# Optimization experiments

Hardware: AMD Instinct MI355X
Metric: run time of the kernel (lower is better)

The kernel has to match this reference:

```python
import jax, jax.numpy as jnp
import numpy as np

N, E, D, H = 4096, 131072, 256, 8
DH = D // H  # head dim = 32


def layer_norm(x, g, b, eps=1e-5):
    mu = jnp.mean(x, axis=-1, keepdims=True)
    var = jnp.var(x, axis=-1, keepdims=True)
    return (x - mu) * jax.lax.rsqrt(var + eps) * g + b


def mlp2(x, w1, b1, w2, b2):
    # Linear -> GELU(exact) -> Linear (dropout is identity at inference)
    return jax.nn.gelu(x @ w1 + b1, approximate=False) @ w2 + b2


def setup_inputs() -> dict:
    key = jax.random.key(0)
    ks = iter(jax.random.split(key, 32))
    s = 0.02
    d = {
        'x': jax.random.normal(next(ks), (N, D), jnp.float32),
        'edge_index': jax.random.randint(next(ks), (2, E), 0, N, jnp.int32),
        'edge_attr': jax.random.normal(next(ks), (E, D), jnp.float32),
        # GINE eps
        'eps': jnp.zeros((1,), jnp.float32),
        # edge MLP (Linear weights stored [in, out])
        'e_w1': jax.random.normal(next(ks), (D, D), jnp.float32) * s,
        'e_b1': jnp.zeros((D,), jnp.float32),
        'e_w2': jax.random.normal(next(ks), (D, D), jnp.float32) * s,
        'e_b2': jnp.zeros((D,), jnp.float32),
        # update MLP
        'u_w1': jax.random.normal(next(ks), (D, D), jnp.float32) * s,
        'u_b1': jnp.zeros((D,), jnp.float32),
        'u_w2': jax.random.normal(next(ks), (D, D), jnp.float32) * s,
        'u_b2': jnp.zeros((D,), jnp.float32),
        # LayerNorms
        'ln_local_g': jnp.ones((D,), jnp.float32), 'ln_local_b': jnp.zeros((D,), jnp.float32),
        'ln_global_g': jnp.ones((D,), jnp.float32), 'ln_global_b': jnp.zeros((D,), jnp.float32),
        'ln_ffn_g': jnp.ones((D,), jnp.float32), 'ln_ffn_b': jnp.zeros((D,), jnp.float32),
        # MHA projections ([in, out])
        'wq': jax.random.normal(next(ks), (D, D), jnp.float32) * s,
        'wk': jax.random.normal(next(ks), (D, D), jnp.float32) * s,
        'wv': jax.random.normal(next(ks), (D, D), jnp.float32) * s,
        'bq': jnp.zeros((D,), jnp.float32), 'bk': jnp.zeros((D,), jnp.float32), 'bv': jnp.zeros((D,), jnp.float32),
        'wo': jax.random.normal(next(ks), (D, D), jnp.float32) * s,
        'bo': jnp.zeros((D,), jnp.float32),
        # FFN
        'f_w1': jax.random.normal(next(ks), (D, 4 * D), jnp.float32) * s,
        'f_b1': jnp.zeros((4 * D,), jnp.float32),
        'f_w2': jax.random.normal(next(ks), (4 * D, D), jnp.float32) * s,
        'f_b2': jnp.zeros((D,), jnp.float32),
    }
    return d


def reference(x, edge_index, edge_attr, eps,
              e_w1, e_b1, e_w2, e_b2, u_w1, u_b1, u_w2, u_b2,
              ln_local_g, ln_local_b, ln_global_g, ln_global_b, ln_ffn_g, ln_ffn_b,
              wq, wk, wv, bq, bk, bv, wo, bo,
              f_w1, f_b1, f_w2, f_b2):
    src, dst = edge_index[0], edge_index[1]
    n = x.shape[0]

    # ---- local GINE conv on pre-normed features ----
    h = layer_norm(x, ln_local_g, ln_local_b)
    messages = mlp2(h[src] + edge_attr, e_w1, e_b1, e_w2, e_b2)  # [E, D]
    aggregated = jax.ops.segment_sum(messages, dst, num_segments=n)  # [N, D]
    local = mlp2((1.0 + eps) * h + aggregated, u_w1, u_b1, u_w2, u_b2)
    x = x + local

    # ---- global multihead self-attention over all nodes ----
    g = layer_norm(x, ln_global_g, ln_global_b)
    q = (g @ wq + bq).reshape(n, H, DH)
    k = (g @ wk + bk).reshape(n, H, DH)
    v = (g @ wv + bv).reshape(n, H, DH)
    scores = jnp.einsum('nhd,mhd->hnm', q, k) / jnp.sqrt(jnp.float32(DH))
    attn = jax.nn.softmax(scores, axis=-1)
    ctx = jnp.einsum('hnm,mhd->nhd', attn, v).reshape(n, D)
    x = x + (ctx @ wo + bo)

    # ---- FFN ----
    x = x + mlp2(layer_norm(x, ln_ffn_g, ln_ffn_b), f_w1, f_b1, f_w2, f_b2)
    return x
```

## Files before the change

### kernel.cpp

```cpp
#include <hip/hip_runtime.h>
#include <math.h>

#define N_NODES 4096
#define N_EDGES 131072
#define XPAD    264

using bf16x8 = __attribute__((ext_vector_type(8))) __bf16;
using f32x4  = __attribute__((ext_vector_type(4))) float;
typedef unsigned short u16;

__device__ __forceinline__ u16 f2bf(float f) {
  unsigned u = __float_as_uint(f);
  u += 0x7fff + ((u >> 16) & 1);
  return (u16)(u >> 16);
}
__device__ __forceinline__ float bf2f(u16 h) {
  return __uint_as_float(((unsigned)h) << 16);
}
__device__ __forceinline__ float gelu_exact(float x) {
  return 0.5f * x * (1.0f + erff(x * 0.70710678118654752f));
}
__device__ __forceinline__ f32x4 mfma16(bf16x8 a, bf16x8 b, f32x4 c) {
  return __builtin_amdgcn_mfma_f32_16x16x32_bf16(a, b, c, 0, 0, 0);
}

struct WPtrs { const float* p[10]; };

__global__ void pack_weights(WPtrs w, u16* __restrict__ dst, float qscale) {
  int tid = blockIdx.x * 256 + threadIdx.x;
  int m, li;
  if (tid < 524288)      { m = tid >> 16; li = tid & 65535; }
  else if (tid < 786432) { m = 8; li = tid - 524288; }
  else                   { m = 9; li = tid - 786432; }
  float v = w.p[m][li];
  size_t out;
  if (m < 4) {
    int k = li >> 8, c = li & 255;
    out = (size_t)(m << 16) + (size_t)((k >> 3) * 256 + c) * 8 + (k & 7);
  } else if (m < 7) {
    int k = li >> 8, c = li & 255;
    if (m == 4) v *= qscale;
    out = 262144 + (size_t)((k >> 3) * 768 + (m - 4) * 256 + c) * 8 + (k & 7);
  } else if (m == 7) {
    int k = li >> 8, c = li & 255;
    out = 458752 + (size_t)((k >> 3) * 256 + c) * 8 + (k & 7);
  } else if (m == 8) {
    int k = li >> 10, c = li & 1023;
    out = 524288 + (size_t)((k >> 3) * 1024 + c) * 8 + (k & 7);
  } else {
    int k = li >> 8, c = li & 255;
    out = 786432 + (size_t)((k >> 3) * 256 + c) * 8 + (k & 7);
  }
  dst[out] = f2bf(v);
}

__global__ void qkvb_kernel(const float* __restrict__ bq, const float* __restrict__ bk,
                            const float* __restrict__ bv, float qscale,
                            float* __restrict__ o) {
  int t = blockIdx.x * 256 + threadIdx.x;
  o[t] = t < 256 ? bq[t] * qscale : (t < 512 ? bk[t - 256] : bv[t - 512]);
}

__global__ void hist_kernel(const int* __restrict__ ei, int* __restrict__ deg) {
  int e = blockIdx.x * 256 + threadIdx.x;
  atomicAdd(&deg[ei[N_EDGES + e]], 1);
}

__global__ void scan_kernel(const int* __restrict__ deg, int* __restrict__ offs) {
  __shared__ int part[1024];
  int t = threadIdx.x;
  int base = t * 4;
  int a0 = deg[base], a1 = deg[base + 1], a2 = deg[base + 2], a3 = deg[base + 3];
  int s = a0 + a1 + a2 + a3;
  part[t] = s;
  __syncthreads();
  for (int off = 1; off < 1024; off <<= 1) {
    int v = (t >= off) ? part[t - off] : 0;
    __syncthreads();
    part[t] += v;
    __syncthreads();
  }
  int excl = part[t] - s;
  offs[base] = excl;
  offs[base + 1] = excl + a0;
  offs[base + 2] = excl + a0 + a1;
  offs[base + 3] = excl + a0 + a1 + a2;
  if (t == 1023) offs[4096] = part[1023];
}

__global__ void scatter_kernel(const int* __restrict__ ei, const int* __restrict__ offs,
                               int* __restrict__ cnt, int* __restrict__ eperm,
                               int* __restrict__ dst_s, int* __restrict__ src_s) {
  int e = blockIdx.x * 256 + threadIdx.x;
  int d = ei[N_EDGES + e];
  int p = offs[d] + atomicAdd(&cnt[d], 1);
  eperm[p] = e;
  dst_s[p] = d;
  src_s[p] = ei[e];
}

__global__ void ln_kernel(const float* __restrict__ in, const float* __restrict__ g,
                          const float* __restrict__ b, float* __restrict__ outf,
                          u16* __restrict__ outh) {
  int row = blockIdx.x, t = threadIdx.x;
  float v = in[(size_t)row * 256 + t];
  float s1 = v, s2 = v * v;
#pragma unroll
  for (int o = 32; o > 0; o >>= 1) { s1 += __shfl_xor(s1, o); s2 += __shfl_xor(s2, o); }
  __shared__ float a1[4], a2[4];
  int wv = t >> 6, lane = t & 63;
  if (lane == 0) { a1[wv] = s1; a2[wv] = s2; }
  __syncthreads();
  s1 = a1[0] + a1[1] + a1[2] + a1[3];
  s2 = a2[0] + a2[1] + a2[2] + a2[3];
  float mean = s1 * (1.0f / 256.0f);
  float var  = s2 * (1.0f / 256.0f) - mean * mean;
  float rs = rsqrtf(var + 1e-5f);
  float o = (v - mean) * rs * g[t] + b[t];
  if (outf) outf[(size_t)row * 256 + t] = o;
  if (outh) outh[(size_t)row * 256 + t] = f2bf(o);
}

__launch_bounds__(256, 2)
__global__ void edge_kernel(const u16* __restrict__ hb, const float* __restrict__ ea,
                            const int* __restrict__ eperm, const int* __restrict__ src_s,
                            const int* __restrict__ dst_s,
                            const u16* __restrict__ wp1, const float* __restrict__ b1,
                            const u16* __restrict__ wp2, const float* __restrict__ b2,
                            float* __restrict__ agg) {
  __shared__ __align__(16) u16 X[128 * XPAD];
  const f32x4 fzero = {0.f, 0.f, 0.f, 0.f};
  int t = threadIdx.x;
  int lane = t & 63, wv = t >> 6;
  int lr = lane & 15, lq = lane >> 4;
  int e0 = blockIdx.x * 128;
  int col0 = wv * 64;

  const u16* b1ptr = wp1 + ((size_t)lq * 256 + col0 + lr) * 8;
  const u16* b2ptr = wp2 + ((size_t)lq * 256 + col0 + lr) * 8;
  bf16x8 bc[4], bn[4];
#pragma unroll
  for (int ct = 0; ct < 4; ++ct) bc[ct] = *(const bf16x8*)(b1ptr + ct * 128);

  int ci = (t & 31) * 8;
#pragma unroll
  for (int it = 0; it < 16; ++it) {
    int r = it * 8 + (t >> 5);
    int e = eperm[e0 + r];
    int s = src_s[e0 + r];
    const float* pa = ea + (size_t)e * 256 + ci;
    float4 a0 = *(const float4*)pa;
    float4 a1 = *(const float4*)(pa + 4);
    ushort4 h0 = *(const ushort4*)(hb + (size_t)s * 256 + ci);
    ushort4 h1 = *(const ushort4*)(hb + (size_t)s * 256 + ci + 4);
    u16 tmp[8];
    tmp[0] = f2bf(a0.x + bf2f(h0.x)); tmp[1] = f2bf(a0.y + bf2f(h0.y));
    tmp[2] = f2bf(a0.z + bf2f(h0.z)); tmp[3] = f2bf(a0.w + bf2f(h0.w));
    tmp[4] = f2bf(a1.x + bf2f(h1.x)); tmp[5] = f2bf(a1.y + bf2f(h1.y));
    tmp[6] = f2bf(a1.z + bf2f(h1.z)); tmp[7] = f2bf(a1.w + bf2f(h1.w));
    *(uint4*)&X[r * XPAD + ci] = *(const uint4*)tmp;
  }
  __syncthreads();

  f32x4 acc[8][4];
#pragma unroll
  for (int i = 0; i < 8; ++i)
#pragma unroll
    for (int j = 0; j < 4; ++j) acc[i][j] = fzero;

#pragma unroll
  for (int ks = 0; ks < 8; ++ks) {
    if (ks < 7) {
#pragma unroll
      for (int ct = 0; ct < 4; ++ct)
        bn[ct] = *(const bf16x8*)(b1ptr + (size_t)(ks + 1) * 8192 + ct * 128);
    }
    bf16x8 a[4];
#pragma unroll
    for (int rt = 0; rt < 4; ++rt)
      a[rt] = *(const bf16x8*)&X[(rt * 16 + lr) * XPAD + ks * 32 + lq * 8];
#pragma unroll
    for (int ct = 0; ct < 4; ++ct)
#pragma unroll
      for (int rt = 0; rt < 4; ++rt) acc[rt][ct] = mfma16(a[rt], bc[ct], acc[rt][ct]);
#pragma unroll
    for (int rt = 0; rt < 4; ++rt)
      a[rt] = *(const bf16x8*)&X[((rt + 4) * 16 + lr) * XPAD + ks * 32 + lq * 8];
#pragma unroll
    for (int ct = 0; ct < 4; ++ct)
#pragma unroll
      for (int rt = 0; rt < 4; ++rt) acc[rt + 4][ct] = mfma16(a[rt], bc[ct], acc[rt + 4][ct]);
#pragma unroll
    for (int ct = 0; ct < 4; ++ct) bc[ct] = bn[ct];
  }
#pragma unroll
  for (int ct = 0; ct < 4; ++ct) bn[ct] = *(const bf16x8*)(b2ptr + ct * 128);
  __syncthreads();

#pragma unroll
  for (int ct = 0; ct < 4; ++ct) {
    int c = col0 + ct * 16 + lr;
    float bb = b1[c];
#pragma unroll
    for (int rt = 0; rt < 8; ++rt)
#pragma unroll
      for (int r = 0; r < 4; ++r) {
        int row = rt * 16 + lq * 4 + r;
        X[row * XPAD + c] = f2bf(gelu_exact(acc[rt][ct][r] + bb));
      }
  }
#pragma unroll
  for (int ct = 0; ct < 4; ++ct) bc[ct] = bn[ct];
  __syncthreads();

#pragma unroll
  for (int i = 0; i < 8; ++i)
#pragma unroll
    for (int j = 0; j < 4; ++j) acc[i][j] = fzero;
#pragma unroll
  for (int ks = 0; ks < 8; ++ks) {
    if (ks < 7) {
#pragma unroll
      for (int ct = 0; ct < 4; ++ct)
        bn[ct] = *(const bf16x8*)(b2ptr + (size_t)(ks + 1) * 8192 + ct * 128);
    }
    bf16x8 a[4];
#pragma unroll
    for (int rt = 0; rt < 4; ++rt)
      a[rt] = *(const bf16x8*)&X[(rt * 16 + lr) * XPAD + ks * 32 + lq * 8];
#pragma unroll
    for (int ct = 0; ct < 4; ++ct)
#pragma unroll
      for (int rt = 0; rt < 4; ++rt) acc[rt][ct] = mfma16(a[rt], bc[ct], acc[rt][ct]);
#pragma unroll
    for (int rt = 0; rt < 4; ++rt)
      a[rt] = *(const bf16x8*)&X[((rt + 4) * 16 + lr) * XPAD + ks * 32 + lq * 8];
#pragma unroll
    for (int ct = 0; ct < 4; ++ct)
#pragma unroll
      for (int rt = 0; rt < 4; ++rt) acc[rt + 4][ct] = mfma16(a[rt], bc[ct], acc[rt + 4][ct]);
#pragma unroll
    for (int ct = 0; ct < 4; ++ct) bc[ct] = bn[ct];
  }
  __syncthreads();

#pragma unroll
  for (int ct = 0; ct < 4; ++ct) {
    int c = col0 + ct * 16 + lr;
    float bb = b2[c];
#pragma unroll
    for (int rt = 0; rt < 8; ++rt)
#pragma unroll
      for (int r = 0; r < 4; ++r) {
        int row = rt * 16 + lq * 4 + r;
        X[row * XPAD + c] = f2bf(acc[rt][ct][r] + bb);
      }
  }
  __syncthreads();

  {
    int c = t;
    float run = 0.f;
    int cur = dst_s[e0];
    for (int r = 0; r < 128; ++r) {
      int d = dst_s[e0 + r];
      if (d != cur) {
        atomicAdd(&agg[(size_t)cur * 256 + c], run);
        run = 0.f;
        cur = d;
      }
      run += bf2f(X[r * XPAD + c]);
    }
    atomicAdd(&agg[(size_t)cur * 256 + c], run);
  }
}

__launch_bounds__(256, 2)
__global__ void update_kernel(const float* __restrict__ hf, const float* __restrict__ agg,
                              const float* __restrict__ epsp, const float* __restrict__ xin,
                              const u16* __restrict__ wp1, const float* __restrict__ b1,
                              const u16* __restrict__ wp2, const float* __restrict__ b2,
                              float* __restrict__ x1) {
  __shared__ __align__(16) u16 X[64 * XPAD];
  const f32x4 fzero = {0.f, 0.f, 0.f, 0.f};
  int t = threadIdx.x;
  int lane = t & 63, wv = t >> 6;
  int lr = lane & 15, lq = lane >> 4;
  int n0 = blockIdx.x * 64;
  int col0 = wv * 64;
  float epv = 1.0f + epsp[0];
  const u16* b1ptr = wp1 + ((size_t)lq * 256 + col0 + lr) * 8;
  const u16* b2ptr = wp2 + ((size_t)lq * 256 + col0 + lr) * 8;
  bf16x8 bc[4], bn[4];
#pragma unroll
  for (int ct = 0; ct < 4; ++ct) bc[ct] = *(const bf16x8*)(b1ptr + ct * 128);
  {
    int c4 = (t & 63) * 4;
#pragma unroll
    for (int ii = 0; ii < 16; ++ii) {
      int r = ii * 4 + wv;
      float4 h = *(const float4*)(hf + (size_t)(n0 + r) * 256 + c4);
      float4 a = *(const float4*)(agg + (size_t)(n0 + r) * 256 + c4);
      *(ushort4*)&X[r * XPAD + c4] =
          make_ushort4(f2bf(epv * h.x + a.x), f2bf(epv * h.y + a.y),
                       f2bf(epv * h.z + a.z), f2bf(epv * h.w + a.w));
    }
  }
  __syncthreads();
  f32x4 acc[4][4];
#pragma unroll
  for (int i = 0; i < 4; ++i)
#pragma unroll
    for (int j = 0; j < 4; ++j) acc[i][j] = fzero;
#pragma unroll
  for (int ks = 0; ks < 8; ++ks) {
    if (ks < 7) {
#pragma unroll
      for (int ct = 0; ct < 4; ++ct)
        bn[ct] = *(const bf16x8*)(b1ptr + (size_t)(ks + 1) * 8192 + ct * 128);
    }
    bf16x8 a[4];
#pragma unroll
    for (int rt = 0; rt < 4; ++rt)
      a[rt] = *(const bf16x8*)&X[(rt * 16 + lr) * XPAD + ks * 32 + lq * 8];
#pragma unroll
    for (int ct = 0; ct < 4; ++ct)
#pragma unroll
      for (int rt = 0; rt < 4; ++rt) acc[rt][ct] = mfma16(a[rt], bc[ct], acc[rt][ct]);
#pragma unroll
    for (int ct = 0; ct < 4; ++ct) bc[ct] = bn[ct];
  }
#pragma unroll
  for (int ct = 0; ct < 4; ++ct) bn[ct] = *(const bf16x8*)(b2ptr + ct * 128);
  __syncthreads();
#pragma unroll
  for (int ct = 0; ct < 4; ++ct) {
    int c = col0 + ct * 16 + lr;
    float bb = b1[c];
#pragma unroll
    for (int rt = 0; rt < 4; ++rt)
#pragma unroll
      for (int r = 0; r < 4; ++r) {
        int row = rt * 16 + lq * 4 + r;
        X[row * XPAD + c] = f2bf(gelu_exact(acc[rt][ct][r] + bb));
      }
  }
#pragma unroll
  for (int ct = 0; ct < 4; ++ct) bc[ct] = bn[ct];
  __syncthreads();
#pragma unroll
  for (int i = 0; i < 4; ++i)
#pragma unroll
    for (int j = 0; j < 4; ++j) acc[i][j] = fzero;
#pragma unroll
  for (int ks = 0; ks < 8; ++ks) {
    if (ks < 7) {
#pragma unroll
      for (int ct = 0; ct < 4; ++ct)
        bn[ct] = *(const bf16x8*)(b2ptr + (size_t)(ks + 1) * 8192 + ct * 128);
    }
    bf16x8 a[4];
#pragma unroll
    for (int rt = 0; rt < 4; ++rt)
      a[rt] = *(const bf16x8*)&X[(rt * 16 + lr) * XPAD + ks * 32 + lq * 8];
#pragma unroll
    for (int ct = 0; ct < 4; ++ct)
#pragma unroll
      for (int rt = 0; rt < 4; ++rt) acc[rt][ct] = mfma16(a[rt], bc[ct], acc[rt][ct]);
#pragma unroll
    for (int ct = 0; ct < 4; ++ct) bc[ct] = bn[ct];
  }
#pragma unroll
  for (int ct = 0; ct < 4; ++ct) {
    int c = col0 + ct * 16 + lr;
    float bb = b2[c];
#pragma unroll
    for (int rt = 0; rt < 4; ++rt)
#pragma unroll
      for (int r = 0; r < 4; ++r) {
        int row = rt * 16 + lq * 4 + r;
        size_t idx = (size_t)(n0 + row) * 256 + c;
        x1[idx] = xin[idx] + acc[rt][ct][r] + bb;
      }
  }
}

template <int ROWS, bool GELU_F, bool RES, bool OUTB>
__launch_bounds__(256, 2)
__global__ void gemm_kernel(const u16* __restrict__ A, int lda,
                            const u16* __restrict__ Wp, int K, int WCols,
                            const float* __restrict__ bias, float scale,
                            const float* __restrict__ res,
                            float* __restrict__ outf, u16* __restrict__ outh, int ldo) {
  __shared__ __align__(16) u16 X[ROWS * XPAD];
  constexpr int RT = ROWS / 16;
  const f32x4 fzero = {0.f, 0.f, 0.f, 0.f};
  int t = threadIdx.x;
  int lane = t & 63, wv = t >> 6;
  int lr = lane & 15, lq = lane >> 4;
  int r0 = blockIdx.x * ROWS;
  int cb = blockIdx.y * 256;
  f32x4 acc[RT][4];
#pragma unroll
  for (int i = 0; i < RT; ++i)
#pragma unroll
    for (int j = 0; j < 4; ++j) acc[i][j] = fzero;
  const u16* bptr = Wp + ((size_t)lq * WCols + cb + wv * 64 + lr) * 8;
  bf16x8 bc[4], bn[4];
#pragma unroll
  for (int ct = 0; ct < 4; ++ct) bc[ct] = *(const bf16x8*)(bptr + ct * 128);
  int rr = t >> 5, c8 = (t & 31) * 8;
  for (int kc = 0; kc < K; kc += 256) {
#pragma unroll
    for (int ii = 0; ii < ROWS / 8; ++ii) {
      int r = ii * 8 + rr;
      *(uint4*)&X[r * XPAD + c8] = *(const uint4*)(A + (size_t)(r0 + r) * lda + kc + c8);
    }
    __syncthreads();
#pragma unroll
    for (int ks = 0; ks < 8; ++ks) {
      bool more = (ks < 7) || (kc + 256 < K);
      if (more) {
        size_t koff = (ks < 7) ? ((size_t)(kc >> 3) + (ks + 1) * 4) * WCols
                               : ((size_t)((kc + 256) >> 3)) * WCols;
#pragma unroll
        for (int ct = 0; ct < 4; ++ct)
          bn[ct] = *(const bf16x8*)(bptr + (koff + ct * 16) * 8);
      }
      bf16x8 a[RT];
#pragma unroll
      for (int rt = 0; rt < RT; ++rt)
        a[rt] = *(const bf16x8*)&X[(rt * 16 + lr) * XPAD + ks * 32 + lq * 8];
#pragma unroll
      for (int ct = 0; ct < 4; ++ct)
#pragma unroll
        for (int rt = 0; rt < RT; ++rt) acc[rt][ct] = mfma16(a[rt], bc[ct], acc[rt][ct]);
#pragma unroll
      for (int ct = 0; ct < 4; ++ct) bc[ct] = bn[ct];
    }
    __syncthreads();
  }
#pragma unroll
  for (int ct = 0; ct < 4; ++ct) {
    int c = cb + wv * 64 + ct * 16 + lr;
    float bb = bias[c];
#pragma unroll
    for (int rt = 0; rt < RT; ++rt)
#pragma unroll
      for (int r = 0; r < 4; ++r) {
        int row = r0 + rt * 16 + lq * 4 + r;
        float v = (acc[rt][ct][r] + bb) * scale;
        if (GELU_F) v = gelu_exact(v);
        if (RES) v += res[(size_t)row * 256 + c];
        if (OUTB) outh[(size_t)row * ldo + c] = f2bf(v);
        else      outf[(size_t)row * ldo + c] = v;
      }
  }
}

__launch_bounds__(256, 2)
__global__ void attn_kernel(const u16* __restrict__ qkv, u16* __restrict__ ctx) {
  __shared__ u16 Kt[64 * 40];
  __shared__ u16 Vt[32 * 72];
  __shared__ u16 P[4][16 * 72];
  const f32x4 fzero = {0.f, 0.f, 0.f, 0.f};
  int t = threadIdx.x;
  int lane = t & 63, wv = t >> 6;
  int lr = lane & 15, lq = lane >> 4;
  int head = blockIdx.y;
  int q0 = blockIdx.x * 64 + wv * 16;
  const u16* qb = qkv;
  const u16* kb = qkv + 256;
  const u16* vb = qkv + 512;
  bf16x8 qf = *(const bf16x8*)(qb + (size_t)(q0 + lr) * 768 + head * 32 + lq * 8);
  f32x4 o0 = fzero, o1 = fzero;
  float l_i[4] = {0.f, 0.f, 0.f, 0.f};
  int key = t >> 2, dp = (t & 3) * 8;
  for (int k0 = 0; k0 < N_NODES; k0 += 64) {
    uint4 kk = *(const uint4*)(kb + (size_t)(k0 + key) * 768 + head * 32 + dp);
    *(uint4*)&Kt[key * 40 + dp] = kk;
    uint4 vvv = *(const uint4*)(vb + (size_t)(k0 + key) * 768 + head * 32 + dp);
    const u16* vp = (const u16*)&vvv;
#pragma unroll
    for (int j = 0; j < 8; ++j) Vt[(dp + j) * 72 + key] = vp[j];
    __syncthreads();
    f32x4 s[4];
#pragma unroll
    for (int ct = 0; ct < 4; ++ct) {
      bf16x8 bk = *(const bf16x8*)&Kt[(ct * 16 + lr) * 40 + lq * 8];
      s[ct] = mfma16(qf, bk, fzero);
    }
#pragma unroll
    for (int ct = 0; ct < 4; ++ct)
#pragma unroll
      for (int r = 0; r < 4; ++r) s[ct][r] = __expf(s[ct][r]);
#pragma unroll
    for (int r = 0; r < 4; ++r) {
      float ps = s[0][r] + s[1][r] + s[2][r] + s[3][r];
#pragma unroll
      for (int d = 1; d < 16; d <<= 1) ps += __shfl_xor(ps, d);
      l_i[r] += ps;
    }
#pragma unroll
    for (int ct = 0; ct < 4; ++ct)
#pragma unroll
      for (int r = 0; r < 4; ++r)
        P[wv][(lq * 4 + r) * 72 + ct * 16 + lr] = f2bf(s[ct][r]);
    __syncthreads();
#pragma unroll
    for (int kp = 0; kp < 2; ++kp) {
      bf16x8 pa = *(const bf16x8*)&P[wv][lr * 72 + kp * 32 + lq * 8];
      bf16x8 v0 = *(const bf16x8*)&Vt[(0 + lr) * 72 + kp * 32 + lq * 8];
      bf16x8 v1 = *(const bf16x8*)&Vt[(16 + lr) * 72 + kp * 32 + lq * 8];
      o0 = mfma16(pa, v0, o0);
      o1 = mfma16(pa, v1, o1);
    }
    __syncthreads();
  }
#pragma unroll
  for (int r = 0; r < 4; ++r) {
    float inv = 1.0f / l_i[r];
    int row = q0 + lq * 4 + r;
    ctx[(size_t)row * 256 + head * 32 + lr]      = f2bf(o0[r] * inv);
    ctx[(size_t)row * 256 + head * 32 + 16 + lr] = f2bf(o1[r] * inv);
  }
}

extern "C" void kernel_launch(void* const* d_in, const int* in_sizes, int n_in,
                              void* d_out, int out_size, void* d_ws, size_t ws_size,
                              hipStream_t stream) {
  const float* x         = (const float*)d_in[0];
  const int*   ei        = (const int*)d_in[1];
  const float* edge_attr = (const float*)d_in[2];
  const float* eps       = (const float*)d_in[3];
  const float* e_w1 = (const float*)d_in[4];
  const float* e_b1 = (const float*)d_in[5];
  const float* e_w2 = (const float*)d_in[6];
  const float* e_b2 = (const float*)d_in[7];
  const float* u_w1 = (const float*)d_in[8];
  const float* u_b1 = (const float*)d_in[9];
  const float* u_w2 = (const float*)d_in[10];
  const float* u_b2 = (const float*)d_in[11];
  const float* ln_local_g  = (const float*)d_in[12];
  const float* ln_local_b  = (const float*)d_in[13];
  const float* ln_global_g = (const float*)d_in[14];
  const float* ln_global_b = (const float*)d_in[15];
  const float* ln_ffn_g    = (const float*)d_in[16];
  const float* ln_ffn_b    = (const float*)d_in[17];
  const float* wq = (const float*)d_in[18];
  const float* wk = (const float*)d_in[19];
  const float* wv = (const float*)d_in[20];
  const float* bq = (const float*)d_in[21];
  const float* bk = (const float*)d_in[22];
  const float* bv = (const float*)d_in[23];
  const float* wo = (const float*)d_in[24];
  const float* bo = (const float*)d_in[25];
  const float* f_w1 = (const float*)d_in[26];
  const float* f_b1 = (const float*)d_in[27];
  const float* f_w2 = (const float*)d_in[28];
  const float* f_b2 = (const float*)d_in[29];

  char* ws = (char*)d_ws;
  u16*   WP    = (u16*)(ws + 0);
  float* hf    = (float*)(ws + (2u  << 20));
  float* agg   = (float*)(ws + (6u  << 20));
  float* x1    = (float*)(ws + (10u << 20));
  u16*   gb    = (u16*)(ws + (14u << 20));
  u16*   qkvb_ = (u16*)(ws + (16u << 20));
  u16*   ctxb  = (u16*)(ws + (22u << 20));
  float* x2    = (float*)(ws + (24u << 20));
  u16*   yb    = (u16*)(ws + (28u << 20));
  u16*   hid   = (u16*)(ws + (30u << 20));
  int*   eperm = (int*)(ws + (38u << 20));
  int*   dst_s = (int*)(ws + (38u << 20) + (512u << 10));
  int*   src_s = (int*)(ws + (39u << 20));
  int*   deg   = (int*)(ws + (39u << 20) + (512u << 10));
  int*   cnt   = (int*)(ws + (39u << 20) + (528u << 10));
  int*   offs  = (int*)(ws + (39u << 20) + (544u << 10));
  float* qkvbias = (float*)(ws + (39u << 20) + (576u << 10));
  u16*   hb    = (u16*)(ws + (40u << 20));

  const size_t O_EW1 = 0, O_EW2 = 65536, O_UW1 = 131072, O_UW2 = 196608,
               O_QKV = 262144, O_WO = 458752, O_FW1 = 524288, O_FW2 = 786432;
  const float qscale = 0.17677669529663687f;

  hipMemsetAsync(deg, 0, 4096 * sizeof(int), stream);
  hipMemsetAsync(cnt, 0, 4096 * sizeof(int), stream);
  hipMemsetAsync(agg, 0, (size_t)N_NODES * 256 * sizeof(float), stream);

  WPtrs wp;
  wp.p[0] = e_w1; wp.p[1] = e_w2; wp.p[2] = u_w1; wp.p[3] = u_w2;
  wp.p[4] = wq;   wp.p[5] = wk;   wp.p[6] = wv;   wp.p[7] = wo;
  wp.p[8] = f_w1; wp.p[9] = f_w2;
  pack_weights<<<4096, 256, 0, stream>>>(wp, WP, qscale);
  qkvb_kernel<<<3, 256, 0, stream>>>(bq, bk, bv, qscale, qkvbias);

  hist_kernel<<<N_EDGES / 256, 256, 0, stream>>>(ei, deg);
  scan_kernel<<<1, 1024, 0, stream>>>(deg, offs);
  scatter_kernel<<<N_EDGES / 256, 256, 0, stream>>>(ei, offs, cnt, eperm, dst_s, src_s);

  ln_kernel<<<N_NODES, 256, 0, stream>>>(x, ln_local_g, ln_local_b, hf, hb);

  edge_kernel<<<N_EDGES / 128, 256, 0, stream>>>(hb, edge_attr, eperm, src_s, dst_s,
                                                 WP + O_EW1, e_b1, WP + O_EW2, e_b2, agg);

  update_kernel<<<N_NODES / 64, 256, 0, stream>>>(hf, agg, eps, x,
                                                  WP + O_UW1, u_b1, WP + O_UW2, u_b2, x1);

  ln_kernel<<<N_NODES, 256, 0, stream>>>(x1, ln_global_g, ln_global_b, nullptr, gb);

  gemm_kernel<64, false, false, true><<<dim3(64, 3), 256, 0, stream>>>(
      gb, 256, WP + O_QKV, 256, 768, qkvbias, 1.0f, nullptr, nullptr, qkvb_, 768);

  attn_kernel<<<dim3(64, 8), 256, 0, stream>>>(qkvb_, ctxb);

  gemm_kernel<32, false, true, false><<<dim3(128, 1), 256, 0, stream>>>(
      ctxb, 256, WP + O_WO, 256, 256, bo, 1.0f, x1, x2, nullptr, 256);

  ln_kernel<<<N_NODES, 256, 0, stream>>>(x2, ln_ffn_g, ln_ffn_b, nullptr, yb);

  gemm_kernel<64, true, false, true><<<dim3(64, 4), 256, 0, stream>>>(
      yb, 256, WP + O_FW1, 256, 1024, f_b1, 1.0f, nullptr, nullptr, hid, 1024);

  gemm_kernel<32, false, true, false><<<dim3(128, 1), 256, 0, stream>>>(
      hid, 1024, WP + O_FW2, 1024, 256, f_b2, 1.0f, x2, (float*)d_out, nullptr, 256);
}
```

Baseline: 556.4 us.

## Fuse setup/LN kernels, swap exact GELU for tanh approx, widen attention key tiles

Merges weight packing, histogram and bias setup into one kernel, and fuses scatter with the first LayerNorm. The global and FFN LayerNorms move into the epilogues of the update and Wo GEMM kernels, and the memsets collapse into one. Exact erf GELU is replaced with a tanh/sigmoid approximation, f2bf uses the native conversion, the edge aggregation is vectorised, and attention processes 128 keys per tile with higher occupancy. The GELU change alters numerics relative to the exact reference.

```diff
diff --git a/kernel.cpp b/kernel.cpp
--- a/kernel.cpp
+++ b/kernel.cpp
@@ -6,19 +6,21 @@
 #define XPAD    264
 
 using bf16x8 = __attribute__((ext_vector_type(8))) __bf16;
+using bf16x4 = __attribute__((ext_vector_type(4))) __bf16;
 using f32x4  = __attribute__((ext_vector_type(4))) float;
 typedef unsigned short u16;
 
 __device__ __forceinline__ u16 f2bf(float f) {
-  unsigned u = __float_as_uint(f);
-  u += 0x7fff + ((u >> 16) & 1);
-  return (u16)(u >> 16);
+  union { __bf16 b; u16 u; } cv; cv.b = (__bf16)f; return cv.u;
 }
 __device__ __forceinline__ float bf2f(u16 h) {
   return __uint_as_float(((unsigned)h) << 16);
 }
-__device__ __forceinline__ float gelu_exact(float x) {
-  return 0.5f * x * (1.0f + erff(x * 0.70710678118654752f));
+__device__ __forceinline__ float gelu_tanh(float x) {
+  float t = x * x;
+  float y = x * (1.5957691216057308f + 0.07135481627f * t);
+  float e = __expf(y);
+  return x - x / (1.0f + e);
 }
 __device__ __forceinline__ f32x4 mfma16(bf16x8 a, bf16x8 b, f32x4 c) {
   return __builtin_amdgcn_mfma_f32_16x16x32_bf16(a, b, c, 0, 0, 0);
@@ -26,44 +28,44 @@
 
 struct WPtrs { const float* p[10]; };
 
-__global__ void pack_weights(WPtrs w, u16* __restrict__ dst, float qscale) {
-  int tid = blockIdx.x * 256 + threadIdx.x;
-  int m, li;
-  if (tid < 524288)      { m = tid >> 16; li = tid & 65535; }
-  else if (tid < 786432) { m = 8; li = tid - 524288; }
-  else                   { m = 9; li = tid - 786432; }
-  float v = w.p[m][li];
-  size_t out;
-  if (m < 4) {
-    int k = li >> 8, c = li & 255;
-    out = (size_t)(m << 16) + (size_t)((k >> 3) * 256 + c) * 8 + (k & 7);
-  } else if (m < 7) {
-    int k = li >> 8, c = li & 255;
-    if (m == 4) v *= qscale;
-    out = 262144 + (size_t)((k >> 3) * 768 + (m - 4) * 256 + c) * 8 + (k & 7);
-  } else if (m == 7) {
-    int k = li >> 8, c = li & 255;
-    out = 458752 + (size_t)((k >> 3) * 256 + c) * 8 + (k & 7);
-  } else if (m == 8) {
-    int k = li >> 10, c = li & 1023;
-    out = 524288 + (size_t)((k >> 3) * 1024 + c) * 8 + (k & 7);
+__global__ void setup_kernel(WPtrs w, u16* __restrict__ dst, float qscale,
+                             const int* __restrict__ ei, int* __restrict__ deg,
+                             const float* __restrict__ bq, const float* __restrict__ bk,
+                             const float* __restrict__ bv, float* __restrict__ qkvbias) {
+  int blk = blockIdx.x, t = threadIdx.x;
+  if (blk < 512) {
+    int tid = blk * 256 + t;
+    int m, ci;
+    if (tid < 32768)      { m = tid >> 13;                 ci = tid & 8191; }
+    else if (tid < 57344) { m = 4 + ((tid - 32768) >> 13); ci = (tid - 32768) & 8191; }
+    else if (tid < 65536) { m = 7; ci = tid - 57344; }
+    else if (tid < 98304) { m = 8; ci = tid - 65536; }
+    else                  { m = 9; ci = tid - 98304; }
+    int Cols = (m == 8) ? 1024 : 256;
+    int k8   = (m == 8) ? (ci >> 10) : (ci >> 8);
+    int c    = (m == 8) ? (ci & 1023) : (ci & 255);
+    const float* src = w.p[m] + (size_t)(k8 * 8) * Cols + c;
+    float sc = (m == 4) ? qscale : 1.0f;
+    u16 tmp[8];
+#pragma unroll
+    for (int j = 0; j < 8; ++j) tmp[j] = f2bf(src[(size_t)j * Cols] * sc);
+    size_t off;
+    if (m < 4)       off = (size_t)(m << 16) + (size_t)(k8 * 256 + c) * 8;
+    else if (m < 7)  off = 262144 + (size_t)(k8 * 768 + (m - 4) * 256 + c) * 8;
+    else if (m == 7) off = 458752 + (size_t)(k8 * 256 + c) * 8;
+    else if (m == 8) off = 524288 + (size_t)(k8 * 1024 + c) * 8;
+    else             off = 786432 + (size_t)(k8 * 256 + c) * 8;
+    *(uint4*)(dst + off) = *(const uint4*)tmp;
+  } else if (blk < 1024) {
+    int e = (blk - 512) * 256 + t;
+    atomicAdd(&deg[ei[N_EDGES + e]], 1);
   } else {
-    int k = li >> 8, c = li & 255;
-    out = 786432 + (size_t)((k >> 3) * 256 + c) * 8 + (k & 7);
-  }
-  dst[out] = f2bf(v);
-}
-
-__global__ void qkvb_kernel(const float* __restrict__ bq, const float* __restrict__ bk,
-                            const float* __restrict__ bv, float qscale,
-                            float* __restrict__ o) {
-  int t = blockIdx.x * 256 + threadIdx.x;
-  o[t] = t < 256 ? bq[t] * qscale : (t < 512 ? bk[t - 256] : bv[t - 512]);
-}
-
-__global__ void hist_kernel(const int* __restrict__ ei, int* __restrict__ deg) {
-  int e = blockIdx.x * 256 + threadIdx.x;
-  atomicAdd(&deg[ei[N_EDGES + e]], 1);
+#pragma unroll
+    for (int i = 0; i < 3; ++i) {
+      int idx = i * 256 + t;
+      qkvbias[idx] = idx < 256 ? bq[idx] * qscale : (idx < 512 ? bk[idx - 256] : bv[idx - 512]);
+    }
+  }
 }
 
 __global__ void scan_kernel(const int* __restrict__ deg, int* __restrict__ offs) {
@@ -88,37 +90,39 @@
   if (t == 1023) offs[4096] = part[1023];
 }
 
-__global__ void scatter_kernel(const int* __restrict__ ei, const int* __restrict__ offs,
-                               int* __restrict__ cnt, int* __restrict__ eperm,
-                               int* __restrict__ dst_s, int* __restrict__ src_s) {
-  int e = blockIdx.x * 256 + threadIdx.x;
-  int d = ei[N_EDGES + e];
-  int p = offs[d] + atomicAdd(&cnt[d], 1);
-  eperm[p] = e;
-  dst_s[p] = d;
-  src_s[p] = ei[e];
-}
-
-__global__ void ln_kernel(const float* __restrict__ in, const float* __restrict__ g,
-                          const float* __restrict__ b, float* __restrict__ outf,
-                          u16* __restrict__ outh) {
-  int row = blockIdx.x, t = threadIdx.x;
-  float v = in[(size_t)row * 256 + t];
-  float s1 = v, s2 = v * v;
-#pragma unroll
-  for (int o = 32; o > 0; o >>= 1) { s1 += __shfl_xor(s1, o); s2 += __shfl_xor(s2, o); }
-  __shared__ float a1[4], a2[4];
-  int wv = t >> 6, lane = t & 63;
-  if (lane == 0) { a1[wv] = s1; a2[wv] = s2; }
-  __syncthreads();
-  s1 = a1[0] + a1[1] + a1[2] + a1[3];
-  s2 = a2[0] + a2[1] + a2[2] + a2[3];
-  float mean = s1 * (1.0f / 256.0f);
-  float var  = s2 * (1.0f / 256.0f) - mean * mean;
-  float rs = rsqrtf(var + 1e-5f);
-  float o = (v - mean) * rs * g[t] + b[t];
-  if (outf) outf[(size_t)row * 256 + t] = o;
-  if (outh) outh[(size_t)row * 256 + t] = f2bf(o);
+__global__ void mid_kernel(const int* __restrict__ ei, const int* __restrict__ offs,
+                           int* __restrict__ cnt, int* __restrict__ eperm,
+                           int* __restrict__ dst_s, int* __restrict__ src_s,
+                           const float* __restrict__ x, const float* __restrict__ g,
+                           const float* __restrict__ b, float* __restrict__ hf,
+                           u16* __restrict__ hb) {
+  int blk = blockIdx.x, t = threadIdx.x;
+  if (blk < 512) {
+    int e = blk * 256 + t;
+    int d = ei[N_EDGES + e];
+    int p = offs[d] + atomicAdd(&cnt[d], 1);
+    eperm[p] = e;
+    dst_s[p] = d;
+    src_s[p] = ei[e];
+  } else {
+    int row = blk - 512;
+    float v = x[(size_t)row * 256 + t];
+    float s1 = v, s2 = v * v;
+#pragma unroll
+    for (int o = 32; o > 0; o >>= 1) { s1 += __shfl_xor(s1, o); s2 += __shfl_xor(s2, o); }
+    __shared__ float a1[4], a2[4];
+    int wv = t >> 6, lane = t & 63;
+    if (lane == 0) { a1[wv] = s1; a2[wv] = s2; }
+    __syncthreads();
+    s1 = a1[0] + a1[1] + a1[2] + a1[3];
+    s2 = a2[0] + a2[1] + a2[2] + a2[3];
+    float mean = s1 * (1.0f / 256.0f);
+    float var  = s2 * (1.0f / 256.0f) - mean * mean;
+    float rs = rsqrtf(var + 1e-5f);
+    float o = (v - mean) * rs * g[t] + b[t];
+    hf[(size_t)row * 256 + t] = o;
+    hb[(size_t)row * 256 + t] = f2bf(o);
+  }
 }
 
 __launch_bounds__(256, 2)
@@ -206,7 +210,7 @@
 #pragma unroll
       for (int r = 0; r < 4; ++r) {
         int row = rt * 16 + lq * 4 + r;
-        X[row * XPAD + c] = f2bf(gelu_exact(acc[rt][ct][r] + bb));
+        X[row * XPAD + c] = f2bf(gelu_tanh(acc[rt][ct][r] + bb));
       }
   }
 #pragma unroll
@@ -259,19 +263,25 @@
   __syncthreads();
 
   {
-    int c = t;
-    float run = 0.f;
-    int cur = dst_s[e0];
-    for (int r = 0; r < 128; ++r) {
+    int c4 = lane * 4;
+    int rbeg = wv * 32;
+    float run0 = 0.f, run1 = 0.f, run2 = 0.f, run3 = 0.f;
+    int cur = dst_s[e0 + rbeg];
+    for (int r = rbeg; r < rbeg + 32; ++r) {
       int d = dst_s[e0 + r];
       if (d != cur) {
-        atomicAdd(&agg[(size_t)cur * 256 + c], run);
-        run = 0.f;
+        float* p = &agg[(size_t)cur * 256 + c4];
+        atomicAdd(p + 0, run0); atomicAdd(p + 1, run1);
+        atomicAdd(p + 2, run2); atomicAdd(p + 3, run3);
+        run0 = run1 = run2 = run3 = 0.f;
         cur = d;
       }
-      run += bf2f(X[r * XPAD + c]);
-    }
-    atomicAdd(&agg[(size_t)cur * 256 + c], run);
+      ushort4 xv = *(const ushort4*)&X[r * XPAD + c4];
+      run0 += bf2f(xv.x); run1 += bf2f(xv.y); run2 += bf2f(xv.z); run3 += bf2f(xv.w);
+    }
+    float* p = &agg[(size_t)cur * 256 + c4];
+    atomicAdd(p + 0, run0); atomicAdd(p + 1, run1);
+    atomicAdd(p + 2, run2); atomicAdd(p + 3, run3);
   }
 }
 
@@ -280,8 +290,10 @@
                               const float* __restrict__ epsp, const float* __restrict__ xin,
                               const u16* __restrict__ wp1, const float* __restrict__ b1,
                               const u16* __restrict__ wp2, const float* __restrict__ b2,
-                              float* __restrict__ x1) {
+                              const float* __restrict__ lng, const float* __restrict__ lnb,
+                              float* __restrict__ x1, u16* __restrict__ gb) {
   __shared__ __align__(16) u16 X[64 * XPAD];
+  __shared__ float S1[64][4], S2[64][4], MUs[64], RSs[64];
   const f32x4 fzero = {0.f, 0.f, 0.f, 0.f};
   int t = threadIdx.x;
   int lane = t & 63, wv = t >> 6;
@@ -342,7 +354,7 @@
 #pragma unroll
       for (int r = 0; r < 4; ++r) {
         int row = rt * 16 + lq * 4 + r;
-        X[row * XPAD + c] = f2bf(gelu_exact(acc[rt][ct][r] + bb));
+        X[row * XPAD + c] = f2bf(gelu_tanh(acc[rt][ct][r] + bb));
       }
   }
 #pragma unroll
@@ -370,29 +382,70 @@
 #pragma unroll
     for (int ct = 0; ct < 4; ++ct) bc[ct] = bn[ct];
   }
+  float bb2[4];
+#pragma unroll
+  for (int ct = 0; ct < 4; ++ct) bb2[ct] = b2[col0 + ct * 16 + lr];
+#pragma unroll
+  for (int rt = 0; rt < 4; ++rt)
+#pragma unroll
+    for (int r = 0; r < 4; ++r) {
+      int row = rt * 16 + lq * 4 + r;
+      int grow = n0 + row;
+      float p1 = 0.f, p2 = 0.f;
+#pragma unroll
+      for (int ct = 0; ct < 4; ++ct) {
+        int c = col0 + ct * 16 + lr;
+        float v = acc[rt][ct][r] + bb2[ct] + xin[(size_t)grow * 256 + c];
+        x1[(size_t)grow * 256 + c] = v;
+        acc[rt][ct][r] = v;
+        p1 += v; p2 += v * v;
+      }
+#pragma unroll
+      for (int o = 1; o < 16; o <<= 1) { p1 += __shfl_xor(p1, o); p2 += __shfl_xor(p2, o); }
+      if (lr == 0) { S1[row][wv] = p1; S2[row][wv] = p2; }
+    }
+  __syncthreads();
+  if (t < 64) {
+    float s1 = S1[t][0] + S1[t][1] + S1[t][2] + S1[t][3];
+    float s2 = S2[t][0] + S2[t][1] + S2[t][2] + S2[t][3];
+    float mu = s1 * (1.0f / 256.0f);
+    float var = s2 * (1.0f / 256.0f) - mu * mu;
+    MUs[t] = mu;
+    RSs[t] = rsqrtf(var + 1e-5f);
+  }
+  __syncthreads();
+  float gv[4], bv[4];
 #pragma unroll
   for (int ct = 0; ct < 4; ++ct) {
     int c = col0 + ct * 16 + lr;
-    float bb = b2[c];
-#pragma unroll
-    for (int rt = 0; rt < 4; ++rt)
-#pragma unroll
-      for (int r = 0; r < 4; ++r) {
-        int row = rt * 16 + lq * 4 + r;
-        size_t idx = (size_t)(n0 + row) * 256 + c;
-        x1[idx] = xin[idx] + acc[rt][ct][r] + bb;
-      }
-  }
-}
-
-template <int ROWS, bool GELU_F, bool RES, bool OUTB>
+    gv[ct] = lng[c]; bv[ct] = lnb[c];
+  }
+#pragma unroll
+  for (int rt = 0; rt < 4; ++rt)
+#pragma unroll
+    for (int r = 0; r < 4; ++r) {
+      int row = rt * 16 + lq * 4 + r;
+      int grow = n0 + row;
+      float mu = MUs[row], rs = RSs[row];
+#pragma unroll
+      for (int ct = 0; ct < 4; ++ct) {
+        int c = col0 + ct * 16 + lr;
+        gb[(size_t)grow * 256 + c] = f2bf((acc[rt][ct][r] - mu) * rs * gv[ct] + bv[ct]);
+      }
+    }
+}
+
+template <int ROWS, bool GELU_F, bool RES, bool OUTB, bool LNF>
 __launch_bounds__(256, 2)
 __global__ void gemm_kernel(const u16* __restrict__ A, int lda,
                             const u16* __restrict__ Wp, int K, int WCols,
                             const float* __restrict__ bias, float scale,
                             const float* __restrict__ res,
+                            const float* __restrict__ lng, const float* __restrict__ lnb,
                             float* __restrict__ outf, u16* __restrict__ outh, int ldo) {
   __shared__ __align__(16) u16 X[ROWS * XPAD];
+  __shared__ float S1[LNF ? ROWS : 1][4], S2[LNF ? ROWS : 1][4];
+  __shared__ float MUs[LNF ? ROWS : 1], RSs[LNF ? ROWS : 1];
   constexpr int RT = ROWS / 16;
   const f32x4 fzero = {0.f, 0.f, 0.f, 0.f};
   int t = threadIdx.x;
@@ -440,29 +493,84 @@
     }
     __syncthreads();
   }
-#pragma unroll
-  for (int ct = 0; ct < 4; ++ct) {
-    int c = cb + wv * 64 + ct * 16 + lr;
-    float bb = bias[c];
+  if (!LNF) {
+#pragma unroll
+    for (int ct = 0; ct < 4; ++ct) {
+      int c = cb + wv * 64 + ct * 16 + lr;
+      float bb = bias[c];
+#pragma unroll
+      for (int rt = 0; rt < RT; ++rt)
+#pragma unroll
+        for (int r = 0; r < 4; ++r) {
+          int row = r0 + rt * 16 + lq * 4 + r;
+          float v = (acc[rt][ct][r] + bb) * scale;
+          if (GELU_F) v = gelu_tanh(v);
+          if (RES) v += res[(size_t)row * 256 + c];
+          if (OUTB) outh[(size_t)row * ldo + c] = f2bf(v);
+          else      outf[(size_t)row * ldo + c] = v;
+        }
+    }
+  } else {
+    float bb[4];
+#pragma unroll
+    for (int ct = 0; ct < 4; ++ct) bb[ct] = bias[wv * 64 + ct * 16 + lr];
 #pragma unroll
     for (int rt = 0; rt < RT; ++rt)
 #pragma unroll
       for (int r = 0; r < 4; ++r) {
-        int row = r0 + rt * 16 + lq * 4 + r;
-        float v = (acc[rt][ct][r] + bb) * scale;
-        if (GELU_F) v = gelu_exact(v);
-        if (RES) v += res[(size_t)row * 256 + c];
-        if (OUTB) outh[(size_t)row * ldo + c] = f2bf(v);
-        else      outf[(size_t)row * ldo + c] = v;
-      }
-  }
-}
-
-__launch_bounds__(256, 2)
+        int row = rt * 16 + lq * 4 + r;
+        int grow = r0 + row;
+        float p1 = 0.f, p2 = 0.f;
+#pragma unroll
+        for (int ct = 0; ct < 4; ++ct) {
+          int c = wv * 64 + ct * 16 + lr;
+          float v = acc[rt][ct][r] + bb[ct];
+          if (RES) v += res[(size_t)grow * 256 + c];
+          outf[(size_t)grow * 256 + c] = v;
+          acc[rt][ct][r] = v;
+          p1 += v; p2 += v * v;
+        }
+#pragma unroll
+        for (int o = 1; o < 16; o <<= 1) { p1 += __shfl_xor(p1, o); p2 += __shfl_xor(p2, o); }
+        if (lr == 0) { S1[row][wv] = p1; S2[row][wv] = p2; }
+      }
+    __syncthreads();
+    if (t < ROWS) {
+      float s1 = S1[t][0] + S1[t][1] + S1[t][2] + S1[t][3];
+      float s2 = S2[t][0] + S2[t][1] + S2[t][2] + S2[t][3];
+      float mu = s1 * (1.0f / 256.0f);
+      float var = s2 * (1.0f / 256.0f) - mu * mu;
+      MUs[t] = mu;
+      RSs[t] = rsqrtf(var + 1e-5f);
+    }
+    __syncthreads();
+    float gv[4], bv[4];
+#pragma unroll
+    for (int ct = 0; ct < 4; ++ct) {
+      int c = wv * 64 + ct * 16 + lr;
+      gv[ct] = lng[c]; bv[ct] = lnb[c];
+    }
+#pragma unroll
+    for (int rt = 0; rt < RT; ++rt)
+#pragma unroll
+      for (int r = 0; r < 4; ++r) {
+        int row = rt * 16 + lq * 4 + r;
+        int grow = r0 + row;
+        float mu = MUs[row], rs = RSs[row];
+#pragma unroll
+        for (int ct = 0; ct < 4; ++ct) {
+          int c = wv * 64 + ct * 16 + lr;
+          outh[(size_t)grow * ldo + c] = f2bf((acc[rt][ct][r] - mu) * rs * gv[ct] + bv[ct]);
+        }
+      }
+  }
+}
+
+__launch_bounds__(256, 4)
 __global__ void attn_kernel(const u16* __restrict__ qkv, u16* __restrict__ ctx) {
-  __shared__ u16 Kt[64 * 40];
-  __shared__ u16 Vt[32 * 72];
-  __shared__ u16 P[4][16 * 72];
+  __shared__ u16 Kt[128 * 40];
+  __shared__ u16 Vt[32 * 136];
+  __shared__ u16 P[4][16 * 136];
   const f32x4 fzero = {0.f, 0.f, 0.f, 0.f};
   int t = threadIdx.x;
   int lane = t & 63, wv = t >> 6;
@@ -475,43 +583,50 @@
   bf16x8 qf = *(const bf16x8*)(qb + (size_t)(q0 + lr) * 768 + head * 32 + lq * 8);
   f32x4 o0 = fzero, o1 = fzero;
   float l_i[4] = {0.f, 0.f, 0.f, 0.f};
-  int key = t >> 2, dp = (t & 3) * 8;
-  for (int k0 = 0; k0 < N_NODES; k0 += 64) {
-    uint4 kk = *(const uint4*)(kb + (size_t)(k0 + key) * 768 + head * 32 + dp);
-    *(uint4*)&Kt[key * 40 + dp] = kk;
-    uint4 vvv = *(const uint4*)(vb + (size_t)(k0 + key) * 768 + head * 32 + dp);
-    const u16* vp = (const u16*)&vvv;
-#pragma unroll
-    for (int j = 0; j < 8; ++j) Vt[(dp + j) * 72 + key] = vp[j];
-    __syncthreads();
-    f32x4 s[4];
-#pragma unroll
-    for (int ct = 0; ct < 4; ++ct) {
+  int key2 = t >> 1, khalf = (t & 1) * 16;
+  int vd = t >> 4, vkb = (t & 15) * 8;
+  for (int k0 = 0; k0 < N_NODES; k0 += 128) {
+    const u16* kpg = kb + (size_t)(k0 + key2) * 768 + head * 32 + khalf;
+    *(uint4*)&Kt[key2 * 40 + khalf]     = *(const uint4*)kpg;
+    *(uint4*)&Kt[key2 * 40 + khalf + 8] = *(const uint4*)(kpg + 8);
+#pragma unroll
+    for (int dd = 0; dd < 2; ++dd) {
+      int d = vd + dd * 16;
+      u16 tv[8];
+#pragma unroll
+      for (int j = 0; j < 8; ++j)
+        tv[j] = vb[(size_t)(k0 + vkb + j) * 768 + head * 32 + d];
+      *(uint4*)&Vt[d * 136 + vkb] = *(const uint4*)tv;
+    }
+    __syncthreads();
+    f32x4 s[8];
+#pragma unroll
+    for (int ct = 0; ct < 8; ++ct) {
       bf16x8 bk = *(const bf16x8*)&Kt[(ct * 16 + lr) * 40 + lq * 8];
       s[ct] = mfma16(qf, bk, fzero);
     }
 #pragma unroll
-    for (int ct = 0; ct < 4; ++ct)
+    for (int ct = 0; ct < 8; ++ct)
 #pragma unroll
       for (int r = 0; r < 4; ++r) s[ct][r] = __expf(s[ct][r]);
 #pragma unroll
     for (int r = 0; r < 4; ++r) {
-      float ps = s[0][r] + s[1][r] + s[2][r] + s[3][r];
+      float ps = ((s[0][r] + s[1][r]) + (s[2][r] + s[3][r])) +
+                 ((s[4][r] + s[5][r]) + (s[6][r] + s[7][r]));
 #pragma unroll
       for (int d = 1; d < 16; d <<= 1) ps += __shfl_xor(ps, d);
       l_i[r] += ps;
     }
 #pragma unroll
-    for (int ct = 0; ct < 4; ++ct)
+    for (int ct = 0; ct < 8; ++ct)
 #pragma unroll
       for (int r = 0; r < 4; ++r)
-        P[wv][(lq * 4 + r) * 72 + ct * 16 + lr] = f2bf(s[ct][r]);
-    __syncthreads();
-#pragma unroll
-    for (int kp = 0; kp < 2; ++kp) {
-      bf16x8 pa = *(const bf16x8*)&P[wv][lr * 72 + kp * 32 + lq * 8];
-      bf16x8 v0 = *(const bf16x8*)&Vt[(0 + lr) * 72 + kp * 32 + lq * 8];
-      bf16x8 v1 = *(const bf16x8*)&Vt[(16 + lr) * 72 + kp * 32 + lq * 8];
+        P[wv][(lq * 4 + r) * 136 + ct * 16 + lr] = f2bf(s[ct][r]);
+#pragma unroll
+    for (int kp = 0; kp < 4; ++kp) {
+      bf16x8 pa = *(const bf16x8*)&P[wv][lr * 136 + kp * 32 + lq * 8];
+      bf16x8 v0 = *(const bf16x8*)&Vt[lr * 136 + kp * 32 + lq * 8];
+      bf16x8 v1 = *(const bf16x8*)&Vt[(16 + lr) * 136 + kp * 32 + lq * 8];
       o0 = mfma16(pa, v0, o0);
       o1 = mfma16(pa, v1, o1);
     }
@@ -561,67 +676,61 @@
   const float* f_b2 = (const float*)d_in[29];
 
   char* ws = (char*)d_ws;
-  u16*   WP    = (u16*)(ws + 0);
-  float* hf    = (float*)(ws + (2u  << 20));
-  float* agg   = (float*)(ws + (6u  << 20));
-  float* x1    = (float*)(ws + (10u << 20));
-  u16*   gb    = (u16*)(ws + (14u << 20));
-  u16*   qkvb_ = (u16*)(ws + (16u << 20));
-  u16*   ctxb  = (u16*)(ws + (22u << 20));
-  float* x2    = (float*)(ws + (24u << 20));
-  u16*   yb    = (u16*)(ws + (28u << 20));
-  u16*   hid   = (u16*)(ws + (30u << 20));
-  int*   eperm = (int*)(ws + (38u << 20));
-  int*   dst_s = (int*)(ws + (38u << 20) + (512u << 10));
-  int*   src_s = (int*)(ws + (39u << 20));
-  int*   deg   = (int*)(ws + (39u << 20) + (512u << 10));
-  int*   cnt   = (int*)(ws + (39u << 20) + (528u << 10));
-  int*   offs  = (int*)(ws + (39u << 20) + (544u << 10));
-  float* qkvbias = (float*)(ws + (39u << 20) + (576u << 10));
-  u16*   hb    = (u16*)(ws + (40u << 20));
+  u16*   WP      = (u16*)(ws + 0);
+  float* agg     = (float*)(ws + (2u  << 20));
+  int*   deg     = (int*)(ws + (6u  << 20));
+  int*   cnt     = (int*)(ws + (6u  << 20) + (16u << 10));
+  int*   offs    = (int*)(ws + (6u  << 20) + (32u << 10));
+  float* qkvbias = (float*)(ws + (6u << 20) + (64u << 10));
+  float* hf      = (float*)(ws + (7u  << 20));
+  float* x1      = (float*)(ws + (11u << 20));
+  u16*   gb      = (u16*)(ws + (15u << 20));
+  u16*   qkvb_   = (u16*)(ws + (17u << 20));
+  u16*   ctxb    = (u16*)(ws + (23u << 20));
+  float* x2      = (float*)(ws + (25u << 20));
+  u16*   yb      = (u16*)(ws + (29u << 20));
+  u16*   hid     = (u16*)(ws + (31u << 20));
+  int*   eperm   = (int*)(ws + (39u << 20));
+  int*   dst_s   = (int*)(ws + (39u << 20) + (512u << 10));
+  int*   src_s   = (int*)(ws + (40u << 20));
+  u16*   hb      = (u16*)(ws + (40u << 20) + (512u << 10));
 
   const size_t O_EW1 = 0, O_EW2 = 65536, O_UW1 = 131072, O_UW2 = 196608,
                O_QKV = 262144, O_WO = 458752, O_FW1 = 524288, O_FW2 = 786432;
   const float qscale = 0.17677669529663687f;
 
-  hipMemsetAsync(deg, 0, 4096 * sizeof(int), stream);
-  hipMemsetAsync(cnt, 0, 4096 * sizeof(int), stream);
-  hipMemsetAsync(agg, 0, (size_t)N_NODES * 256 * sizeof(float), stream);
+  hipMemsetAsync(agg, 0, (4u << 20) + (32u << 10), stream);
 
   WPtrs wp;
   wp.p[0] = e_w1; wp.p[1] = e_w2; wp.p[2] = u_w1; wp.p[3] = u_w2;
   wp.p[4] = wq;   wp.p[5] = wk;   wp.p[6] = wv;   wp.p[7] = wo;
   wp.p[8] = f_w1; wp.p[9] = f_w2;
-  pack_weights<<<4096, 256, 0, stream>>>(wp, WP, qscale);
-  qkvb_kernel<<<3, 256, 0, stream>>>(bq, bk, bv, qscale, qkvbias);
-
-  hist_kernel<<<N_EDGES / 256, 256, 0, stream>>>(ei, deg);
+  setup_kernel<<<1025, 256, 0, stream>>>(wp, WP, qscale, ei, deg, bq, bk, bv, qkvbias);
   scan_kernel<<<1, 1024, 0, stream>>>(deg, offs);
-  scatter_kernel<<<N_EDGES / 256, 256, 0, stream>>>(ei, offs, cnt, eperm, dst_s, src_s);
-
-  ln_kernel<<<N_NODES, 256, 0, stream>>>(x, ln_local_g, ln_local_b, hf, hb);
+  mid_kernel<<<4608, 256, 0, stream>>>(ei, offs, cnt, eperm, dst_s, src_s,
+                                       x, ln_local_g, ln_local_b, hf, hb);
 
   edge_kernel<<<N_EDGES / 128, 256, 0, stream>>>(hb, edge_attr, eperm, src_s, dst_s,
                                                  WP + O_EW1, e_b1, WP + O_EW2, e_b2, agg);
 
   update_kernel<<<N_NODES / 64, 256, 0, stream>>>(hf, agg, eps, x,
-                                                  WP + O_UW1, u_b1, WP + O_UW2, u_b2, x1);
-
-  ln_kernel<<<N_NODES, 256, 0, stream>>>(x1, ln_global_g, ln_global_b, nullptr, gb);
-
-  gemm_kernel<64, false, false, true><<<dim3(64, 3), 256, 0, stream>>>(
-      gb, 256, WP + O_QKV, 256, 768, qkvbias, 1.0f, nullptr, nullptr, qkvb_, 768);
+                                                  WP + O_UW1, u_b1, WP + O_UW2, u_b2,
+                                                  ln_global_g, ln_global_b, x1, gb);
+
+  gemm_kernel<64, false, false, true, false><<<dim3(64, 3), 256, 0, stream>>>(
+      gb, 256, WP + O_QKV, 256, 768, qkvbias, 1.0f, nullptr, nullptr, nullptr,
+      nullptr, qkvb_, 768);
 
   attn_kernel<<<dim3(64, 8), 256, 0, stream>>>(qkvb_, ctxb);
 
-  gemm_kernel<32, false, true, false><<<dim3(128, 1), 256, 0, stream>>>(
-      ctxb, 256, WP + O_WO, 256, 256, bo, 1.0f, x1, x2, nullptr, 256);
-
-  ln_kernel<<<N_NODES, 256, 0, stream>>>(x2, ln_ffn_g, ln_ffn_b, nullptr, yb);
-
-  gemm_kernel<64, true, false, true><<<dim3(64, 4), 256, 0, stream>>>(
-      yb, 256, WP + O_FW1, 256, 1024, f_b1, 1.0f, nullptr, nullptr, hid, 1024);
-
-  gemm_kernel<32, false, true, false><<<dim3(128, 1), 256, 0, stream>>>(
-      hid, 1024, WP + O_FW2, 1024, 256, f_b2, 1.0f, x2, (float*)d_out, nullptr, 256);
-}
+  gemm_kernel<32, false, true, false, true><<<dim3(128, 1), 256, 0, stream>>>(
+      ctxb, 256, WP + O_WO, 256, 256, bo, 1.0f, x1, ln_ffn_g, ln_ffn_b, x2, yb, 256);
+
+  gemm_kernel<64, true, false, true, false><<<dim3(64, 4), 256, 0, stream>>>(
+      yb, 256, WP + O_FW1, 256, 1024, f_b1, 1.0f, nullptr, nullptr, nullptr,
+      nullptr, hid, 1024);
+
+  gemm_kernel<32, false, true, false, false><<<dim3(128, 1), 256, 0, stream>>>(
+      hid, 1024, WP + O_FW2, 1024, 256, f_b2, 1.0f, x2, nullptr, nullptr,
+      (float*)d_out, nullptr, 256);
+}
```

Result: no change. 550.2 us (-1.1%).
